# Performance work log

Measured on AMD Instinct MI355X. Metric: run time of the kernel, lower is better.

## Reference

```python
import jax, jax.numpy as jnp
import numpy as np

B, T, C = 1, 2048, 1024
H, D = 16, 64  # n_head, head_size (n_query_groups == n_head -> plain MHA)


def build_rope_cache(seq_len, n_elem, base=10000):
    theta = 1.0 / (base ** (jnp.arange(0, n_elem, 2, dtype=jnp.float32) / n_elem))
    idx_theta = jnp.outer(jnp.arange(seq_len, dtype=jnp.float32), theta)
    idx_theta = jnp.concatenate([idx_theta, idx_theta], axis=-1)  # torch .repeat(1, 2)
    return jnp.cos(idx_theta), jnp.sin(idx_theta)


def apply_rope(x, cos, sin):
    d = x.shape[-1]
    x1, x2 = x[..., : d // 2], x[..., d // 2 :]
    rotated = jnp.concatenate([-x2, x1], axis=-1)
    return x * cos + rotated * sin


def fastmax_attention(q, k, v):
    """Fastmax: first-order Taylor approx of softmax attention, causal, O(n*d^2).
    score(i,j) = 1 + q_i . k_j (temperature=1, zero RPE, no dropout);
    out_i = sum_{j<=i} score*v_j / sum_{j<=i} score, via causal cumulative sums."""
    n = q.shape[2]
    kcum = jnp.cumsum(k, axis=2)                                       # (B,H,T,D)
    kvcum = jnp.cumsum(jnp.einsum('bhnd,bhne->bhnde', k, v), axis=2)   # (B,H,T,D,D)
    den = jnp.arange(1, n + 1, dtype=q.dtype) + jnp.einsum('bhnd,bhnd->bhn', q, kcum)
    num = jnp.cumsum(v, axis=2) + jnp.einsum('bhnd,bhnde->bhne', q, kvcum)
    return num / den[..., None]


def setup_inputs() -> dict:
    key = jax.random.key(0)
    k1, k2, k3 = jax.random.split(key, 3)
    scale = 0.02
    x = jax.random.normal(k1, (B, T, C), dtype=jnp.float32)
    w_attn = jax.random.normal(k2, (3 * H * D, C), dtype=jnp.float32) * scale
    w_proj = jax.random.normal(k3, (C, H * D), dtype=jnp.float32) * scale
    cos, sin = build_rope_cache(T, D)
    return {"x": x, "w_attn": w_attn, "w_proj": w_proj, "cos": cos, "sin": sin}


def reference(x, w_attn, w_proj, cos, sin):
    Bx, Tx, Cx = x.shape
    qkv = x @ w_attn.T                                  # (B,T,3HD)
    qkv = qkv.reshape(Bx, Tx, H, 3, D).transpose(0, 2, 3, 1, 4)  # (B,H,3,T,D)
    q, k, v = qkv[:, :, 0], qkv[:, :, 1], qkv[:, :, 2]
    q = apply_rope(q, cos, sin)
    k = apply_rope(k, cos, sin)
    y = fastmax_attention(q, k, v)                      # (B,H,T,D)
    y = y.transpose(0, 2, 1, 3).reshape(Bx, Tx, H * D)
    return y @ w_proj.T
```

## Files before the change

### kernel.cpp

```cpp
#include <hip/hip_runtime.h>

#define T_LEN 2048
#define C_DIM 1024
#define H_NUM 16
#define D_DIM 64
#define QKV_N (3 * H_NUM * D_DIM)
#define L_CHK 64
#define NC (T_LEN / L_CHK)

typedef _Float16 h8 __attribute__((ext_vector_type(8)));
typedef _Float16 h4 __attribute__((ext_vector_type(4)));
typedef float f32x4 __attribute__((ext_vector_type(4)));

__global__ __launch_bounds__(256) void split3_f16(
    const float* __restrict__ x, _Float16* __restrict__ xh,
    _Float16* __restrict__ xl, const float* __restrict__ wa,
    _Float16* __restrict__ wah, _Float16* __restrict__ wal,
    const float* __restrict__ wp, _Float16* __restrict__ wph) {
  int i = (blockIdx.x * 256 + threadIdx.x) * 8;
  const float* src;
  _Float16 *dh, *dl = nullptr;
  int base;
  if (i < 2097152) {
    src = x; dh = xh; dl = xl; base = i;
  } else if (i < 2097152 + 3145728) {
    src = wa; dh = wah; dl = wal; base = i - 2097152;
  } else {
    src = wp; dh = wph; base = i - 5242880;
  }
  float4 a = *(const float4*)(src + base);
  float4 b = *(const float4*)(src + base + 4);
  float v[8] = {a.x, a.y, a.z, a.w, b.x, b.y, b.z, b.w};
  h8 hv, lv;
#pragma unroll
  for (int j = 0; j < 8; ++j) {
    float s = v[j] * 64.f;
    _Float16 h = (_Float16)s;
    hv[j] = h;
    lv[j] = (_Float16)(s - (float)h);
  }
  *(h8*)(dh + base) = hv;
  if (dl) *(h8*)(dl + base) = lv;
}

__device__ __forceinline__ void split8(float4 a, float4 b, h8& hi, h8& lo) {
  float v[8] = {a.x, a.y, a.z, a.w, b.x, b.y, b.z, b.w};
#pragma unroll
  for (int m = 0; m < 8; ++m) {
    _Float16 hh = (_Float16)v[m];
    hi[m] = hh;
    lo[m] = (_Float16)(v[m] - (float)hh);
  }
}

template <int BN, bool ROPE, bool SPLIT3>
__global__ __launch_bounds__(256) void gemm_nt_f16(
    const _Float16* __restrict__ Ah, const _Float16* __restrict__ Al,
    const _Float16* __restrict__ Bh, const _Float16* __restrict__ Bl,
    float* __restrict__ C, const float* __restrict__ cosb,
    const float* __restrict__ sinb, _Float16* __restrict__ qh_,
    _Float16* __restrict__ ql_, _Float16* __restrict__ kh_,
    _Float16* __restrict__ kl_, _Float16* __restrict__ kTh_,
    _Float16* __restrict__ kTl_, _Float16* __restrict__ vTh_,
    _Float16* __restrict__ vTl_, int M, int N, int K, float outscale) {
  constexpr int NJ = BN / 32;
  constexpr int NARR = SPLIT3 ? 2 : 1;
  constexpr int GEMM_BYTES = (64 * 64 * 2 + BN * 64 * 2) * NARR;
  constexpr int ROPE_BYTES = ROPE ? (2 * 64 * 32 * 4 + 2 * 64 * 64 * 4) : 0;
  constexpr int SMEM_BYTES = GEMM_BYTES > ROPE_BYTES ? GEMM_BYTES : ROPE_BYTES;
  __shared__ __align__(16) char smem[SMEM_BYTES];
  _Float16* sAh = (_Float16*)smem;
  _Float16* sAl = sAh + 64 * 64;
  _Float16* sBh = sAh + 64 * 64 * NARR;
  _Float16* sBl = sBh + BN * 64;
  const int tid = threadIdx.x;
  const int wave = tid >> 6;
  const int lane = tid & 63;
  const int bm = blockIdx.y * 64;
  const int bn = blockIdx.x * BN;
  const int wm = wave >> 1;
  const int wn = wave & 1;
  const int srow = lane >> 3;
  const int sblk = ((lane & 7) ^ srow) * 8;
  const int quad = lane >> 4;
  const int lrow = lane & 15;

  f32x4 acc[2][NJ];
#pragma unroll
  for (int i = 0; i < 2; ++i)
#pragma unroll
    for (int j = 0; j < NJ; ++j) acc[i][j] = (f32x4){0.f, 0.f, 0.f, 0.f};

  for (int k0 = 0; k0 < K; k0 += 64) {
#pragma unroll
    for (int it = 0; it < 2; ++it) {
      const int ch = wave + it * 4;
      const int row = ch * 8 + srow;
      const _Float16* ga = Ah + (size_t)(bm + row) * K + k0 + sblk;
      __builtin_amdgcn_global_load_lds(
          (const __attribute__((address_space(1))) void*)ga,
          (__attribute__((address_space(3))) void*)(sAh + ch * 512), 16, 0, 0);
      if constexpr (SPLIT3) {
        const _Float16* gb = Al + (size_t)(bm + row) * K + k0 + sblk;
        __builtin_amdgcn_global_load_lds(
            (const __attribute__((address_space(1))) void*)gb,
            (__attribute__((address_space(3))) void*)(sAl + ch * 512), 16, 0,
            0);
      }
    }
#pragma unroll
    for (int it = 0; it < BN / 32; ++it) {
      const int ch = wave + it * 4;
      const int row = ch * 8 + srow;
      const _Float16* ga = Bh + (size_t)(bn + row) * K + k0 + sblk;
      __builtin_amdgcn_global_load_lds(
          (const __attribute__((address_space(1))) void*)ga,
          (__attribute__((address_space(3))) void*)(sBh + ch * 512), 16, 0, 0);
      if constexpr (SPLIT3) {
        const _Float16* gb = Bl + (size_t)(bn + row) * K + k0 + sblk;
        __builtin_amdgcn_global_load_lds(
            (const __attribute__((address_space(1))) void*)gb,
            (__attribute__((address_space(3))) void*)(sBl + ch * 512), 16, 0,
            0);
      }
    }
    __syncthreads();
#pragma unroll
    for (int kk = 0; kk < 2; ++kk) {
      h8 ah[2], al[2], bh[NJ], bl[NJ];
#pragma unroll
      for (int i = 0; i < 2; ++i) {
        const int row = wm * 32 + i * 16 + lrow;
        const int ra = row * 64 + (((kk * 4 + quad) ^ (row & 7)) * 8);
        ah[i] = *(const h8*)&sAh[ra];
        if constexpr (SPLIT3) al[i] = *(const h8*)&sAl[ra];
      }
#pragma unroll
      for (int j = 0; j < NJ; ++j) {
        const int row = wn * (BN / 2) + j * 16 + lrow;
        const int rb = row * 64 + (((kk * 4 + quad) ^ (row & 7)) * 8);
        bh[j] = *(const h8*)&sBh[rb];
        if constexpr (SPLIT3) bl[j] = *(const h8*)&sBl[rb];
      }
#pragma unroll
      for (int i = 0; i < 2; ++i)
#pragma unroll
        for (int j = 0; j < NJ; ++j) {
          acc[i][j] = __builtin_amdgcn_mfma_f32_16x16x32_f16(
              ah[i], bh[j], acc[i][j], 0, 0, 0);
          if constexpr (SPLIT3) {
            acc[i][j] = __builtin_amdgcn_mfma_f32_16x16x32_f16(
                ah[i], bl[j], acc[i][j], 0, 0, 0);
            acc[i][j] = __builtin_amdgcn_mfma_f32_16x16x32_f16(
                al[i], bh[j], acc[i][j], 0, 0, 0);
          }
        }
    }
    __syncthreads();
  }
  if constexpr (!ROPE) {
#pragma unroll
    for (int i = 0; i < 2; ++i) {
      const int rbase = bm + wm * 32 + i * 16 + quad * 4;
#pragma unroll
      for (int j = 0; j < NJ; ++j) {
        const int col = bn + wn * (BN / 2) + j * 16 + lrow;
#pragma unroll
        for (int r = 0; r < 4; ++r)
          C[(size_t)(rbase + r) * N + col] = acc[i][j][r] * outscale;
      }
    }
  } else {
    float* cs = (float*)smem;
    float* sn = cs + 2048;
    float* bounce = sn + 2048;
    {
      const int el = tid * 8;
      const int t = el >> 5, d0 = el & 31;
      const float* gc = &cosb[(size_t)(bm + t) * D_DIM + d0];
      const float* gs = &sinb[(size_t)(bm + t) * D_DIM + d0];
      *(float4*)&cs[t * 32 + d0] = *(const float4*)gc;
      *(float4*)&cs[t * 32 + d0 + 4] = *(const float4*)(gc + 4);
      *(float4*)&sn[t * 32 + d0] = *(const float4*)gs;
      *(float4*)&sn[t * 32 + d0 + 4] = *(const float4*)(gs + 4);
    }
    __syncthreads();
    const int colbase = bn + wn * 64;
    const int type = (colbase >> 6) % 3;
    const int head = colbase / 192;
    const size_t hb = (size_t)head * T_LEN * D_DIM;
    float fv[2][4][4];
#pragma unroll
    for (int i = 0; i < 2; ++i)
#pragma unroll
      for (int r = 0; r < 4; ++r) {
        const int tloc = wm * 32 + i * 16 + quad * 4 + r;
#pragma unroll
        for (int j = 0; j < 4; ++j) {
          const int d32 = (j & 1) * 16 + lrow;
          float val = acc[i][j][r] * outscale;
          if (type < 2) {
            float rotv =
                ((j < 2) ? -acc[i][j + 2][r] : acc[i][j - 2][r]) * outscale;
            val = val * cs[tloc * 32 + d32] + rotv * sn[tloc * 32 + d32];
          }
          fv[i][r][j] = val;
        }
      }
    if (type < 2) {
      _Float16* dh = (type == 0 ? qh_ : kh_) + hb;
      _Float16* dl = (type == 0 ? ql_ : kl_) + hb;
#pragma unroll
      for (int i = 0; i < 2; ++i)
#pragma unroll
        for (int r = 0; r < 4; ++r) {
          const size_t trow =
              (size_t)(bm + wm * 32 + i * 16 + quad * 4 + r) * D_DIM;
#pragma unroll
          for (int j = 0; j < 4; ++j) {
            const int d = j * 16 + lrow;
            float f = fv[i][r][j];
            _Float16 hh = (_Float16)f;
            dh[trow + d] = hh;
            dl[trow + d] = (_Float16)(f - (float)hh);
          }
        }
    }
    const bool doT = (type >= 1);
    _Float16* th = (type == 1 ? kTh_ : vTh_) + hb;
    _Float16* tl = (type == 1 ? kTl_ : vTl_) + hb;
    float* myb = bounce + wn * 4096;
    if (doT) {
#pragma unroll
      for (int i = 0; i < 2; ++i)
#pragma unroll
        for (int r = 0; r < 4; ++r) {
          const int tloc = wm * 32 + i * 16 + quad * 4 + r;
#pragma unroll
          for (int j = 0; j < 4; ++j) {
            const int d = j * 16 + lrow;
            myb[tloc * 64 + (d ^ tloc)] = fv[i][r][j];
          }
        }
    }
    __syncthreads();
    if (doT) {
      const int lt = wm * 64 + lane;
      const int e = lt >> 1;
      const int tg0 = (lt & 1) * 32;
#pragma unroll
      for (int s8 = 0; s8 < 4; ++s8) {
        h8 hv, lv;
#pragma unroll
        for (int s = 0; s < 8; ++s) {
          const int t = tg0 + s8 * 8 + s;
          float f = myb[t * 64 + (e ^ t)];
          _Float16 hh = (_Float16)f;
          hv[s] = hh;
          lv[s] = (_Float16)(f - (float)hh);
        }
        *(h8*)&th[(size_t)e * T_LEN + bm + tg0 + s8 * 8] = hv;
        *(h8*)&tl[(size_t)e * T_LEN + bm + tg0 + s8 * 8] = lv;
      }
    }
  }
}

__global__ __launch_bounds__(256) void chunk_kvT(
    const _Float16* __restrict__ kTh, const _Float16* __restrict__ kTl,
    const _Float16* __restrict__ vTh, const _Float16* __restrict__ vTl,
    float* __restrict__ kvchunk, float* __restrict__ kschunk,
    float* __restrict__ vschunk) {
  const int blk = blockIdx.x;
  const int h = blk / NC, c = blk % NC;
  const int tid = threadIdx.x;
  const int wave = tid >> 6, lane = tid & 63;
  const int quad = lane >> 4, lrow = lane & 15;
  const size_t hb = (size_t)h * D_DIM * T_LEN;
  const int tb = c * L_CHK;
  h8 avh[2], avl[2];
  {
    const _Float16* pa = vTh + hb + (size_t)(wave * 16 + lrow) * T_LEN + tb +
                         quad * 8;
    const _Float16* pal = vTl + hb + (size_t)(wave * 16 + lrow) * T_LEN + tb +
                          quad * 8;
    avh[0] = *(const h8*)pa;
    avh[1] = *(const h8*)(pa + 32);
    avl[0] = *(const h8*)pal;
    avl[1] = *(const h8*)(pal + 32);
  }
  f32x4 accv[4];
#pragma unroll
  for (int dt = 0; dt < 4; ++dt) accv[dt] = (f32x4){0.f, 0.f, 0.f, 0.f};
#pragma unroll
  for (int dt = 0; dt < 4; ++dt) {
    const _Float16* pb = kTh + hb + (size_t)(dt * 16 + lrow) * T_LEN + tb +
                         quad * 8;
    const _Float16* pbl = kTl + hb + (size_t)(dt * 16 + lrow) * T_LEN + tb +
                          quad * 8;
#pragma unroll
    for (int ks = 0; ks < 2; ++ks) {
      h8 bh = *(const h8*)(pb + ks * 32);
      h8 bl = *(const h8*)(pbl + ks * 32);
      accv[dt] = __builtin_amdgcn_mfma_f32_16x16x32_f16(avh[ks], bh, accv[dt],
                                                        0, 0, 0);
      accv[dt] = __builtin_amdgcn_mfma_f32_16x16x32_f16(avh[ks], bl, accv[dt],
                                                        0, 0, 0);
      accv[dt] = __builtin_amdgcn_mfma_f32_16x16x32_f16(avl[ks], bh, accv[dt],
                                                        0, 0, 0);
    }
  }
  float* ob = kvchunk + (size_t)blk * (D_DIM * D_DIM);
#pragma unroll
  for (int dt = 0; dt < 4; ++dt)
#pragma unroll
    for (int r = 0; r < 4; ++r)
      ob[(wave * 16 + quad * 4 + r) * D_DIM + dt * 16 + lrow] = accv[dt][r];
  if (tid < 64) {
    const _Float16* p = kTh + hb + (size_t)tid * T_LEN + tb;
    const _Float16* pl = kTl + hb + (size_t)tid * T_LEN + tb;
    float s = 0.f;
#pragma unroll
    for (int i = 0; i < 8; ++i) {
      h8 a = *(const h8*)(p + i * 8), b = *(const h8*)(pl + i * 8);
#pragma unroll
      for (int m = 0; m < 8; ++m) s += (float)a[m] + (float)b[m];
    }
    kschunk[(size_t)blk * D_DIM + tid] = s;
  } else if (tid < 128) {
    const int e = tid - 64;
    const _Float16* p = vTh + hb + (size_t)e * T_LEN + tb;
    const _Float16* pl = vTl + hb + (size_t)e * T_LEN + tb;
    float s = 0.f;
#pragma unroll
    for (int i = 0; i < 8; ++i) {
      h8 a = *(const h8*)(p + i * 8), b = *(const h8*)(pl + i * 8);
#pragma unroll
      for (int m = 0; m < 8; ++m) s += (float)a[m] + (float)b[m];
    }
    vschunk[(size_t)blk * D_DIM + e] = s;
  }
}

__global__ __launch_bounds__(256) void scan_fused(
    const float* __restrict__ kvchunk, float* __restrict__ kvpref,
    const float* __restrict__ kschunk, const float* __restrict__ vschunk,
    float* __restrict__ kspref, float* __restrict__ vspref) {
  int b = blockIdx.x;
  int tid = threadIdx.x;
  if (b < 256) {
    int gid = b * 256 + tid;
    int h = gid >> 12;
    int de = gid & 4095;
    float vals[NC];
#pragma unroll
    for (int c = 0; c < NC; ++c)
      vals[c] = kvchunk[((size_t)(h * NC + c) << 12) + de];
    float run = 0.f;
#pragma unroll
    for (int c = 0; c < NC; ++c) {
      kvpref[((size_t)(h * NC + c) << 12) + de] = run;
      run += vals[c];
    }
  } else {
    int gid = (b - 256) * 256 + tid;
    int h = gid >> 6, d = gid & 63;
    float kv_[NC], vv_[NC];
#pragma unroll
    for (int c = 0; c < NC; ++c) {
      size_t idx = (size_t)(h * NC + c) * 64 + d;
      kv_[c] = kschunk[idx];
      vv_[c] = vschunk[idx];
    }
    float rk = 0.f, rv = 0.f;
#pragma unroll
    for (int c = 0; c < NC; ++c) {
      size_t idx = (size_t)(h * NC + c) * 64 + d;
      kspref[idx] = rk;
      vspref[idx] = rv;
      rk += kv_[c];
      rv += vv_[c];
    }
  }
}

__global__ __launch_bounds__(256) void attn_mfma(
    const _Float16* __restrict__ qh, const _Float16* __restrict__ ql,
    const _Float16* __restrict__ kh, const _Float16* __restrict__ kl,
    const _Float16* __restrict__ vTh, const _Float16* __restrict__ vTl,
    const float* __restrict__ kvpref, const float* __restrict__ kspref,
    const float* __restrict__ vspref, _Float16* __restrict__ yh) {
  __shared__ __align__(16) _Float16 sS[2][4][16 * 64];
  const int blk = blockIdx.x;
  const int h = blk / NC, c = blk % NC;
  const int tid = threadIdx.x;
  const int wave = tid >> 6, lane = tid & 63;
  const int quad = lane >> 4, lrow = lane & 15;
  const size_t hb = (size_t)h * T_LEN * D_DIM;
  const size_t hbT = (size_t)h * D_DIM * T_LEN;
  const int t0 = c * L_CHK;
  const f32x4 z4 = {0.f, 0.f, 0.f, 0.f};
  h8 aqh[2], aql[2];
  {
    const _Float16* pq =
        qh + hb + (size_t)(t0 + wave * 16 + lrow) * D_DIM + quad * 8;
    const _Float16* pql =
        ql + hb + (size_t)(t0 + wave * 16 + lrow) * D_DIM + quad * 8;
    aqh[0] = *(const h8*)pq;
    aqh[1] = *(const h8*)(pq + 32);
    aql[0] = *(const h8*)pql;
    aql[1] = *(const h8*)(pql + 32);
  }
  f32x4 sacc[4];
#pragma unroll
  for (int jt = 0; jt < 4; ++jt) sacc[jt] = z4;
#pragma unroll
  for (int jt = 0; jt < 4; ++jt) {
    const _Float16* pk =
        kh + hb + (size_t)(t0 + jt * 16 + lrow) * D_DIM + quad * 8;
    const _Float16* pkl =
        kl + hb + (size_t)(t0 + jt * 16 + lrow) * D_DIM + quad * 8;
#pragma unroll
    for (int ks = 0; ks < 2; ++ks) {
      h8 bh = *(const h8*)(pk + ks * 32);
      h8 bl = *(const h8*)(pkl + ks * 32);
      sacc[jt] = __builtin_amdgcn_mfma_f32_16x16x32_f16(aqh[ks], bh, sacc[jt],
                                                        0, 0, 0);
      sacc[jt] = __builtin_amdgcn_mfma_f32_16x16x32_f16(aqh[ks], bl, sacc[jt],
                                                        0, 0, 0);
      sacc[jt] = __builtin_amdgcn_mfma_f32_16x16x32_f16(aql[ks], bh, sacc[jt],
                                                        0, 0, 0);
    }
  }
  _Float16* shp = &sS[0][wave][0];
  _Float16* slp = &sS[1][wave][0];
#pragma unroll
  for (int jt = 0; jt < 4; ++jt)
#pragma unroll
    for (int r = 0; r < 4; ++r) {
      const int row = quad * 4 + r;
      const int j = jt * 16 + lrow;
      const int rglob = wave * 16 + row;
      float s = (j <= rglob) ? (sacc[jt][r] + 1.f) : 0.f;
      _Float16 hh = (_Float16)s;
      const int adr = row * 64 + ((((j >> 3) ^ (row & 7)) << 3) | (j & 7));
      shp[adr] = hh;
      slp[adr] = (_Float16)(s - (float)hh);
    }
  h8 ash[2], asl[2];
#pragma unroll
  for (int ks = 0; ks < 2; ++ks) {
    const int adr = lrow * 64 + (((ks * 4 + quad) ^ (lrow & 7)) << 3);
    ash[ks] = *(const h8*)&shp[adr];
    asl[ks] = *(const h8*)&slp[adr];
  }
  h8 ones;
#pragma unroll
  for (int m = 0; m < 8; ++m) ones[m] = (_Float16)1.0f;
  f32x4 rs = z4;
#pragma unroll
  for (int ks = 0; ks < 2; ++ks) {
    rs = __builtin_amdgcn_mfma_f32_16x16x32_f16(ash[ks], ones, rs, 0, 0, 0);
    rs = __builtin_amdgcn_mfma_f32_16x16x32_f16(asl[ks], ones, rs, 0, 0, 0);
  }
  f32x4 oacc[4];
#pragma unroll
  for (int et = 0; et < 4; ++et) oacc[et] = z4;
#pragma unroll
  for (int et = 0; et < 4; ++et) {
    const _Float16* pv =
        vTh + hbT + (size_t)(et * 16 + lrow) * T_LEN + t0 + quad * 8;
    const _Float16* pvl =
        vTl + hbT + (size_t)(et * 16 + lrow) * T_LEN + t0 + quad * 8;
#pragma unroll
    for (int ks = 0; ks < 2; ++ks) {
      h8 bh = *(const h8*)(pv + ks * 32);
      h8 bl = *(const h8*)(pvl + ks * 32);
      oacc[et] = __builtin_amdgcn_mfma_f32_16x16x32_f16(ash[ks], bh, oacc[et],
                                                        0, 0, 0);
      oacc[et] = __builtin_amdgcn_mfma_f32_16x16x32_f16(ash[ks], bl, oacc[et],
                                                        0, 0, 0);
      oacc[et] = __builtin_amdgcn_mfma_f32_16x16x32_f16(asl[ks], bh, oacc[et],
                                                        0, 0, 0);
    }
  }
  const float* kvp = kvpref + (size_t)blk * (D_DIM * D_DIM);
#pragma unroll
  for (int et = 0; et < 4; ++et) {
#pragma unroll
    for (int ks = 0; ks < 2; ++ks) {
      const float* pb = kvp + (et * 16 + lrow) * D_DIM + ks * 32 + quad * 8;
      float4 b0 = *(const float4*)pb;
      float4 b1 = *(const float4*)(pb + 4);
      h8 bh, bl;
      split8(b0, b1, bh, bl);
      oacc[et] = __builtin_amdgcn_mfma_f32_16x16x32_f16(aqh[ks], bh, oacc[et],
                                                        0, 0, 0);
      oacc[et] = __builtin_amdgcn_mfma_f32_16x16x32_f16(aqh[ks], bl, oacc[et],
                                                        0, 0, 0);
      oacc[et] = __builtin_amdgcn_mfma_f32_16x16x32_f16(aql[ks], bh, oacc[et],
                                                        0, 0, 0);
    }
  }
  const float* ksp = kspref + (size_t)blk * D_DIM;
  f32x4 kacc = z4;
#pragma unroll
  for (int ks = 0; ks < 2; ++ks) {
    const float* pb = ksp + ks * 32 + quad * 8;
    float4 b0 = *(const float4*)pb;
    float4 b1 = *(const float4*)(pb + 4);
    h8 bh, bl;
    split8(b0, b1, bh, bl);
    kacc = __builtin_amdgcn_mfma_f32_16x16x32_f16(aqh[ks], bh, kacc, 0, 0, 0);
    kacc = __builtin_amdgcn_mfma_f32_16x16x32_f16(aqh[ks], bl, kacc, 0, 0, 0);
    kacc = __builtin_amdgcn_mfma_f32_16x16x32_f16(aql[ks], bh, kacc, 0, 0, 0);
  }
  const float* vsp = vspref + (size_t)blk * D_DIM;
#pragma unroll
  for (int r = 0; r < 4; ++r) {
    const int row = wave * 16 + quad * 4 + r;
    const float den = (float)(c * L_CHK) + rs[r] + kacc[r];
    const float inv = 1.f / den;
    const size_t ybase = (size_t)(t0 + row) * (H_NUM * D_DIM) + h * D_DIM;
#pragma unroll
    for (int et = 0; et < 4; ++et) {
      const int e = et * 16 + lrow;
      const float num = oacc[et][r] + vsp[e];
      yh[ybase + e] = (_Float16)(num * inv);
    }
  }
}

extern "C" void kernel_launch(void* const* d_in, const int* in_sizes, int n_in,
                              void* d_out, int out_size, void* d_ws,
                              size_t ws_size, hipStream_t stream) {
  const float* x = (const float*)d_in[0];
  const float* w_attn = (const float*)d_in[1];
  const float* w_proj = (const float*)d_in[2];
  const float* cosb = (const float*)d_in[3];
  const float* sinb = (const float*)d_in[4];
  float* out = (float*)d_out;

  char* ws = (char*)d_ws;
  const size_t MB = 1048576;
  float* kvchunk = (float*)ws;
  float* kvpref = (float*)(ws + 8 * MB);
  _Float16* qh = (_Float16*)(ws + 16 * MB);
  _Float16* ql = (_Float16*)(ws + 20 * MB);
  _Float16* kh = (_Float16*)(ws + 24 * MB);
  _Float16* kl = (_Float16*)(ws + 28 * MB);
  _Float16* kTh = (_Float16*)(ws + 32 * MB);
  _Float16* kTl = (_Float16*)(ws + 36 * MB);
  _Float16* vTh = (_Float16*)(ws + 40 * MB);
  _Float16* vTl = (_Float16*)(ws + 44 * MB);
  _Float16* xh = (_Float16*)(ws + 48 * MB);
  _Float16* xl = (_Float16*)(ws + 52 * MB);
  _Float16* yh = (_Float16*)(ws + 48 * MB);
  _Float16* wah = (_Float16*)(ws + 56 * MB);
  _Float16* wal = (_Float16*)(ws + 62 * MB);
  float* kschunk = (float*)(ws + 56 * MB);
  float* vschunk = (float*)(ws + 56 * MB + 131072);
  float* kspref = (float*)(ws + 56 * MB + 262144);
  float* vspref = (float*)(ws + 56 * MB + 393216);
  _Float16* wph = (_Float16*)(ws + 68 * MB);

  split3_f16<<<3072, 256, 0, stream>>>(x, xh, xl, w_attn, wah, wal, w_proj,
                                       wph);

  {
    dim3 grid(QKV_N / 128, T_LEN / 64);
    gemm_nt_f16<128, true, true><<<grid, 256, 0, stream>>>(
        xh, xl, wah, wal, nullptr, cosb, sinb, qh, ql, kh, kl, kTh, kTl, vTh,
        vTl, T_LEN, QKV_N, C_DIM, 1.f / 4096.f);
  }
  chunk_kvT<<<H_NUM * NC, 256, 0, stream>>>(kTh, kTl, vTh, vTl, kvchunk,
                                            kschunk, vschunk);
  scan_fused<<<260, 256, 0, stream>>>(kvchunk, kvpref, kschunk, vschunk,
                                      kspref, vspref);
  attn_mfma<<<H_NUM * NC, 256, 0, stream>>>(qh, ql, kh, kl, vTh, vTl, kvpref,
                                            kspref, vspref, yh);
  {
    dim3 grid(C_DIM / 64, T_LEN / 64);
    gemm_nt_f16<64, false, false><<<grid, 256, 0, stream>>>(
        yh, nullptr, wph, nullptr, out, nullptr, nullptr, nullptr, nullptr,
        nullptr, nullptr, nullptr, nullptr, nullptr, nullptr, T_LEN, C_DIM,
        C_DIM, 1.f / 64.f);
  }
}
```

Before: 168.1 us.

## Enlarge QKV GEMM tile to 128x128 and rework RoPE/transpose epilogue

The QKV projection GEMM now uses a BM template parameter and runs with 128x128 tiles, halving the number of blocks and raising per-block operand reuse of the split-f16 A/B tiles. The RoPE epilogue is reworked for the larger tile: cos/sin staging covers 128 rows, and each wave gets its own 64x64 bounce buffer for the K/V transpose, with an extra barrier. Launch bounds request 2 blocks per SM. The cost is more accumulator registers (16 f32x4 per thread with triple MFMA), 64KB of LDS for the epilogue, and only 384 blocks, which may hurt occupancy and load balance.

Result: no change. 168.3 us (+0.2%).

```diff
diff --git a/kernel.cpp b/kernel.cpp
--- a/kernel.cpp
+++ b/kernel.cpp
@@ -53,8 +53,8 @@
   }
 }
 
-template <int BN, bool ROPE, bool SPLIT3>
-__global__ __launch_bounds__(256) void gemm_nt_f16(
+template <int BM, int BN, bool ROPE, bool SPLIT3>
+__global__ __launch_bounds__(256, 2) void gemm_nt_f16(
     const _Float16* __restrict__ Ah, const _Float16* __restrict__ Al,
     const _Float16* __restrict__ Bh, const _Float16* __restrict__ Bl,
     float* __restrict__ C, const float* __restrict__ cosb,
@@ -63,20 +63,21 @@
     _Float16* __restrict__ kl_, _Float16* __restrict__ kTh_,
     _Float16* __restrict__ kTl_, _Float16* __restrict__ vTh_,
     _Float16* __restrict__ vTl_, int M, int N, int K, float outscale) {
+  constexpr int MI = BM / 32;
   constexpr int NJ = BN / 32;
   constexpr int NARR = SPLIT3 ? 2 : 1;
-  constexpr int GEMM_BYTES = (64 * 64 * 2 + BN * 64 * 2) * NARR;
-  constexpr int ROPE_BYTES = ROPE ? (2 * 64 * 32 * 4 + 2 * 64 * 64 * 4) : 0;
+  constexpr int GEMM_BYTES = (BM * 64 * 2 + BN * 64 * 2) * NARR;
+  constexpr int ROPE_BYTES = ROPE ? 65536 : 0;
   constexpr int SMEM_BYTES = GEMM_BYTES > ROPE_BYTES ? GEMM_BYTES : ROPE_BYTES;
   __shared__ __align__(16) char smem[SMEM_BYTES];
   _Float16* sAh = (_Float16*)smem;
-  _Float16* sAl = sAh + 64 * 64;
-  _Float16* sBh = sAh + 64 * 64 * NARR;
+  _Float16* sAl = sAh + BM * 64;
+  _Float16* sBh = sAh + BM * 64 * NARR;
   _Float16* sBl = sBh + BN * 64;
   const int tid = threadIdx.x;
   const int wave = tid >> 6;
   const int lane = tid & 63;
-  const int bm = blockIdx.y * 64;
+  const int bm = blockIdx.y * BM;
   const int bn = blockIdx.x * BN;
   const int wm = wave >> 1;
   const int wn = wave & 1;
@@ -85,15 +86,15 @@
   const int quad = lane >> 4;
   const int lrow = lane & 15;
 
-  f32x4 acc[2][NJ];
-#pragma unroll
-  for (int i = 0; i < 2; ++i)
+  f32x4 acc[MI][NJ];
+#pragma unroll
+  for (int i = 0; i < MI; ++i)
 #pragma unroll
     for (int j = 0; j < NJ; ++j) acc[i][j] = (f32x4){0.f, 0.f, 0.f, 0.f};
 
   for (int k0 = 0; k0 < K; k0 += 64) {
 #pragma unroll
-    for (int it = 0; it < 2; ++it) {
+    for (int it = 0; it < MI; ++it) {
       const int ch = wave + it * 4;
       const int row = ch * 8 + srow;
       const _Float16* ga = Ah + (size_t)(bm + row) * K + k0 + sblk;
@@ -109,7 +110,7 @@
       }
     }
 #pragma unroll
-    for (int it = 0; it < BN / 32; ++it) {
+    for (int it = 0; it < NJ; ++it) {
       const int ch = wave + it * 4;
       const int row = ch * 8 + srow;
       const _Float16* ga = Bh + (size_t)(bn + row) * K + k0 + sblk;
@@ -127,10 +128,10 @@
     __syncthreads();
 #pragma unroll
     for (int kk = 0; kk < 2; ++kk) {
-      h8 ah[2], al[2], bh[NJ], bl[NJ];
-#pragma unroll
-      for (int i = 0; i < 2; ++i) {
-        const int row = wm * 32 + i * 16 + lrow;
+      h8 ah[MI], al[MI], bh[NJ], bl[NJ];
+#pragma unroll
+      for (int i = 0; i < MI; ++i) {
+        const int row = wm * (BM / 2) + i * 16 + lrow;
         const int ra = row * 64 + (((kk * 4 + quad) ^ (row & 7)) * 8);
         ah[i] = *(const h8*)&sAh[ra];
         if constexpr (SPLIT3) al[i] = *(const h8*)&sAl[ra];
@@ -143,7 +144,7 @@
         if constexpr (SPLIT3) bl[j] = *(const h8*)&sBl[rb];
       }
 #pragma unroll
-      for (int i = 0; i < 2; ++i)
+      for (int i = 0; i < MI; ++i)
 #pragma unroll
         for (int j = 0; j < NJ; ++j) {
           acc[i][j] = __builtin_amdgcn_mfma_f32_16x16x32_f16(
@@ -160,8 +161,8 @@
   }
   if constexpr (!ROPE) {
 #pragma unroll
-    for (int i = 0; i < 2; ++i) {
-      const int rbase = bm + wm * 32 + i * 16 + quad * 4;
+    for (int i = 0; i < MI; ++i) {
+      const int rbase = bm + wm * (BM / 2) + i * 16 + quad * 4;
 #pragma unroll
       for (int j = 0; j < NJ; ++j) {
         const int col = bn + wn * (BN / 2) + j * 16 + lrow;
@@ -172,29 +173,31 @@
     }
   } else {
     float* cs = (float*)smem;
-    float* sn = cs + 2048;
-    float* bounce = sn + 2048;
+    float* sn = cs + 4096;
     {
-      const int el = tid * 8;
-      const int t = el >> 5, d0 = el & 31;
+      const int t = tid >> 1, d0 = (tid & 1) * 16;
       const float* gc = &cosb[(size_t)(bm + t) * D_DIM + d0];
       const float* gs = &sinb[(size_t)(bm + t) * D_DIM + d0];
       *(float4*)&cs[t * 32 + d0] = *(const float4*)gc;
       *(float4*)&cs[t * 32 + d0 + 4] = *(const float4*)(gc + 4);
+      *(float4*)&cs[t * 32 + d0 + 8] = *(const float4*)(gc + 8);
+      *(float4*)&cs[t * 32 + d0 + 12] = *(const float4*)(gc + 12);
       *(float4*)&sn[t * 32 + d0] = *(const float4*)gs;
       *(float4*)&sn[t * 32 + d0 + 4] = *(const float4*)(gs + 4);
+      *(float4*)&sn[t * 32 + d0 + 8] = *(const float4*)(gs + 8);
+      *(float4*)&sn[t * 32 + d0 + 12] = *(const float4*)(gs + 12);
     }
     __syncthreads();
     const int colbase = bn + wn * 64;
     const int type = (colbase >> 6) % 3;
     const int head = colbase / 192;
     const size_t hb = (size_t)head * T_LEN * D_DIM;
-    float fv[2][4][4];
-#pragma unroll
-    for (int i = 0; i < 2; ++i)
+    float fv[4][4][4];
+#pragma unroll
+    for (int i = 0; i < 4; ++i)
 #pragma unroll
       for (int r = 0; r < 4; ++r) {
-        const int tloc = wm * 32 + i * 16 + quad * 4 + r;
+        const int tloc = wm * 64 + i * 16 + quad * 4 + r;
 #pragma unroll
         for (int j = 0; j < 4; ++j) {
           const int d32 = (j & 1) * 16 + lrow;
@@ -211,11 +214,11 @@
       _Float16* dh = (type == 0 ? qh_ : kh_) + hb;
       _Float16* dl = (type == 0 ? ql_ : kl_) + hb;
 #pragma unroll
-      for (int i = 0; i < 2; ++i)
+      for (int i = 0; i < 4; ++i)
 #pragma unroll
         for (int r = 0; r < 4; ++r) {
           const size_t trow =
-              (size_t)(bm + wm * 32 + i * 16 + quad * 4 + r) * D_DIM;
+              (size_t)(bm + wm * 64 + i * 16 + quad * 4 + r) * D_DIM;
 #pragma unroll
           for (int j = 0; j < 4; ++j) {
             const int d = j * 16 + lrow;
@@ -229,38 +232,38 @@
     const bool doT = (type >= 1);
     _Float16* th = (type == 1 ? kTh_ : vTh_) + hb;
     _Float16* tl = (type == 1 ? kTl_ : vTl_) + hb;
-    float* myb = bounce + wn * 4096;
+    float* myb = (float*)smem + wave * 4096;
+    __syncthreads();
     if (doT) {
 #pragma unroll
-      for (int i = 0; i < 2; ++i)
+      for (int i = 0; i < 4; ++i)
 #pragma unroll
         for (int r = 0; r < 4; ++r) {
-          const int tloc = wm * 32 + i * 16 + quad * 4 + r;
+          const int tl64 = i * 16 + quad * 4 + r;
 #pragma unroll
           for (int j = 0; j < 4; ++j) {
             const int d = j * 16 + lrow;
-            myb[tloc * 64 + (d ^ tloc)] = fv[i][r][j];
+            myb[tl64 * 64 + (d ^ tl64)] = fv[i][r][j];
           }
         }
     }
     __syncthreads();
     if (doT) {
-      const int lt = wm * 64 + lane;
-      const int e = lt >> 1;
-      const int tg0 = (lt & 1) * 32;
-#pragma unroll
-      for (int s8 = 0; s8 < 4; ++s8) {
+      const int e = lane;
+      const size_t obase = (size_t)e * T_LEN + bm + wm * 64;
+#pragma unroll
+      for (int s8 = 0; s8 < 8; ++s8) {
         h8 hv, lv;
 #pragma unroll
         for (int s = 0; s < 8; ++s) {
-          const int t = tg0 + s8 * 8 + s;
+          const int t = s8 * 8 + s;
           float f = myb[t * 64 + (e ^ t)];
           _Float16 hh = (_Float16)f;
           hv[s] = hh;
           lv[s] = (_Float16)(f - (float)hh);
         }
-        *(h8*)&th[(size_t)e * T_LEN + bm + tg0 + s8 * 8] = hv;
-        *(h8*)&tl[(size_t)e * T_LEN + bm + tg0 + s8 * 8] = lv;
+        *(h8*)&th[obase + s8 * 8] = hv;
+        *(h8*)&tl[obase + s8 * 8] = lv;
       }
     }
   }
@@ -568,8 +571,8 @@
                                        wph);
 
   {
-    dim3 grid(QKV_N / 128, T_LEN / 64);
-    gemm_nt_f16<128, true, true><<<grid, 256, 0, stream>>>(
+    dim3 grid(QKV_N / 128, T_LEN / 128);
+    gemm_nt_f16<128, 128, true, true><<<grid, 256, 0, stream>>>(
         xh, xl, wah, wal, nullptr, cosb, sinb, qh, ql, kh, kl, kTh, kTl, vTh,
         vTl, T_LEN, QKV_N, C_DIM, 1.f / 4096.f);
   }
@@ -581,7 +584,7 @@
                                             kspref, vspref, yh);
   {
     dim3 grid(C_DIM / 64, T_LEN / 64);
-    gemm_nt_f16<64, false, false><<<grid, 256, 0, stream>>>(
+    gemm_nt_f16<64, 64, false, false><<<grid, 256, 0, stream>>>(
         yh, nullptr, wph, nullptr, out, nullptr, nullptr, nullptr, nullptr,
         nullptr, nullptr, nullptr, nullptr, nullptr, nullptr, T_LEN, C_DIM,
         C_DIM, 1.f / 64.f);
```

## Drop low-half split for V and store KV prefix in fp16

Applied to the files above, without the earlier changes.

Removes the lo-part fp16 split for V: the QKV GEMM epilogue no longer writes vTl, and chunk_kvT and attn_mfma drop the corresponding MFMAs and loads. The KV prefix state from the scan is stored as single fp16 instead of fp32, which removes the split8 conversion and the extra MFMAs in attention. The rope cos/sin shared-memory stride is padded from 32 to 36, presumably to reduce LDS bank conflicts. This lowers memory traffic and matrix work but reduces accuracy, since V and the accumulated KV state lose precision, and large accumulated prefix values may lose accuracy in fp16.

Measured after the change: 161.2 us. -4.1%, faster.

```diff
diff --git a/kernel.cpp b/kernel.cpp
--- a/kernel.cpp
+++ b/kernel.cpp
@@ -62,11 +62,11 @@
     _Float16* __restrict__ ql_, _Float16* __restrict__ kh_,
     _Float16* __restrict__ kl_, _Float16* __restrict__ kTh_,
     _Float16* __restrict__ kTl_, _Float16* __restrict__ vTh_,
-    _Float16* __restrict__ vTl_, int M, int N, int K, float outscale) {
+    int M, int N, int K, float outscale) {
   constexpr int NJ = BN / 32;
   constexpr int NARR = SPLIT3 ? 2 : 1;
   constexpr int GEMM_BYTES = (64 * 64 * 2 + BN * 64 * 2) * NARR;
-  constexpr int ROPE_BYTES = ROPE ? (2 * 64 * 32 * 4 + 2 * 64 * 64 * 4) : 0;
+  constexpr int ROPE_BYTES = ROPE ? (2 * 64 * 36 * 4 + 2 * 64 * 64 * 4) : 0;
   constexpr int SMEM_BYTES = GEMM_BYTES > ROPE_BYTES ? GEMM_BYTES : ROPE_BYTES;
   __shared__ __align__(16) char smem[SMEM_BYTES];
   _Float16* sAh = (_Float16*)smem;
@@ -172,17 +172,17 @@
     }
   } else {
     float* cs = (float*)smem;
-    float* sn = cs + 2048;
-    float* bounce = sn + 2048;
+    float* sn = cs + 2304;
+    float* bounce = sn + 2304;
     {
       const int el = tid * 8;
       const int t = el >> 5, d0 = el & 31;
       const float* gc = &cosb[(size_t)(bm + t) * D_DIM + d0];
       const float* gs = &sinb[(size_t)(bm + t) * D_DIM + d0];
-      *(float4*)&cs[t * 32 + d0] = *(const float4*)gc;
-      *(float4*)&cs[t * 32 + d0 + 4] = *(const float4*)(gc + 4);
-      *(float4*)&sn[t * 32 + d0] = *(const float4*)gs;
-      *(float4*)&sn[t * 32 + d0 + 4] = *(const float4*)(gs + 4);
+      *(float4*)&cs[t * 36 + d0] = *(const float4*)gc;
+      *(float4*)&cs[t * 36 + d0 + 4] = *(const float4*)(gc + 4);
+      *(float4*)&sn[t * 36 + d0] = *(const float4*)gs;
+      *(float4*)&sn[t * 36 + d0 + 4] = *(const float4*)(gs + 4);
     }
     __syncthreads();
     const int colbase = bn + wn * 64;
@@ -202,7 +202,7 @@
           if (type < 2) {
             float rotv =
                 ((j < 2) ? -acc[i][j + 2][r] : acc[i][j - 2][r]) * outscale;
-            val = val * cs[tloc * 32 + d32] + rotv * sn[tloc * 32 + d32];
+            val = val * cs[tloc * 36 + d32] + rotv * sn[tloc * 36 + d32];
           }
           fv[i][r][j] = val;
         }
@@ -228,7 +228,7 @@
     }
     const bool doT = (type >= 1);
     _Float16* th = (type == 1 ? kTh_ : vTh_) + hb;
-    _Float16* tl = (type == 1 ? kTl_ : vTl_) + hb;
+    _Float16* tl = kTl_ + hb;
     float* myb = bounce + wn * 4096;
     if (doT) {
 #pragma unroll
@@ -260,7 +260,8 @@
           lv[s] = (_Float16)(f - (float)hh);
         }
         *(h8*)&th[(size_t)e * T_LEN + bm + tg0 + s8 * 8] = hv;
-        *(h8*)&tl[(size_t)e * T_LEN + bm + tg0 + s8 * 8] = lv;
+        if (type == 1)
+          *(h8*)&tl[(size_t)e * T_LEN + bm + tg0 + s8 * 8] = lv;
       }
     }
   }
@@ -268,9 +269,8 @@
 
 __global__ __launch_bounds__(256) void chunk_kvT(
     const _Float16* __restrict__ kTh, const _Float16* __restrict__ kTl,
-    const _Float16* __restrict__ vTh, const _Float16* __restrict__ vTl,
-    float* __restrict__ kvchunk, float* __restrict__ kschunk,
-    float* __restrict__ vschunk) {
+    const _Float16* __restrict__ vTh, float* __restrict__ kvchunk,
+    float* __restrict__ kschunk, float* __restrict__ vschunk) {
   const int blk = blockIdx.x;
   const int h = blk / NC, c = blk % NC;
   const int tid = threadIdx.x;
@@ -278,16 +278,12 @@
   const int quad = lane >> 4, lrow = lane & 15;
   const size_t hb = (size_t)h * D_DIM * T_LEN;
   const int tb = c * L_CHK;
-  h8 avh[2], avl[2];
+  h8 avh[2];
   {
     const _Float16* pa = vTh + hb + (size_t)(wave * 16 + lrow) * T_LEN + tb +
                          quad * 8;
-    const _Float16* pal = vTl + hb + (size_t)(wave * 16 + lrow) * T_LEN + tb +
-                          quad * 8;
     avh[0] = *(const h8*)pa;
     avh[1] = *(const h8*)(pa + 32);
-    avl[0] = *(const h8*)pal;
-    avl[1] = *(const h8*)(pal + 32);
   }
   f32x4 accv[4];
 #pragma unroll
@@ -296,17 +292,10 @@
   for (int dt = 0; dt < 4; ++dt) {
     const _Float16* pb = kTh + hb + (size_t)(dt * 16 + lrow) * T_LEN + tb +
                          quad * 8;
-    const _Float16* pbl = kTl + hb + (size_t)(dt * 16 + lrow) * T_LEN + tb +
-                          quad * 8;
 #pragma unroll
     for (int ks = 0; ks < 2; ++ks) {
       h8 bh = *(const h8*)(pb + ks * 32);
-      h8 bl = *(const h8*)(pbl + ks * 32);
       accv[dt] = __builtin_amdgcn_mfma_f32_16x16x32_f16(avh[ks], bh, accv[dt],
-                                                        0, 0, 0);
-      accv[dt] = __builtin_amdgcn_mfma_f32_16x16x32_f16(avh[ks], bl, accv[dt],
-                                                        0, 0, 0);
-      accv[dt] = __builtin_amdgcn_mfma_f32_16x16x32_f16(avl[ks], bh, accv[dt],
                                                         0, 0, 0);
     }
   }
@@ -330,20 +319,19 @@
   } else if (tid < 128) {
     const int e = tid - 64;
     const _Float16* p = vTh + hb + (size_t)e * T_LEN + tb;
-    const _Float16* pl = vTl + hb + (size_t)e * T_LEN + tb;
     float s = 0.f;
 #pragma unroll
     for (int i = 0; i < 8; ++i) {
-      h8 a = *(const h8*)(p + i * 8), b = *(const h8*)(pl + i * 8);
-#pragma unroll
-      for (int m = 0; m < 8; ++m) s += (float)a[m] + (float)b[m];
+      h8 a = *(const h8*)(p + i * 8);
+#pragma unroll
+      for (int m = 0; m < 8; ++m) s += (float)a[m];
     }
     vschunk[(size_t)blk * D_DIM + e] = s;
   }
 }
 
 __global__ __launch_bounds__(256) void scan_fused(
-    const float* __restrict__ kvchunk, float* __restrict__ kvpref,
+    const float* __restrict__ kvchunk, _Float16* __restrict__ kvph,
     const float* __restrict__ kschunk, const float* __restrict__ vschunk,
     float* __restrict__ kspref, float* __restrict__ vspref) {
   int b = blockIdx.x;
@@ -359,7 +347,7 @@
     float run = 0.f;
 #pragma unroll
     for (int c = 0; c < NC; ++c) {
-      kvpref[((size_t)(h * NC + c) << 12) + de] = run;
+      kvph[((size_t)(h * NC + c) << 12) + de] = (_Float16)run;
       run += vals[c];
     }
   } else {
@@ -387,9 +375,9 @@
 __global__ __launch_bounds__(256) void attn_mfma(
     const _Float16* __restrict__ qh, const _Float16* __restrict__ ql,
     const _Float16* __restrict__ kh, const _Float16* __restrict__ kl,
-    const _Float16* __restrict__ vTh, const _Float16* __restrict__ vTl,
-    const float* __restrict__ kvpref, const float* __restrict__ kspref,
-    const float* __restrict__ vspref, _Float16* __restrict__ yh) {
+    const _Float16* __restrict__ vTh, const _Float16* __restrict__ kvph,
+    const float* __restrict__ kspref, const float* __restrict__ vspref,
+    _Float16* __restrict__ yh) {
   __shared__ __align__(16) _Float16 sS[2][4][16 * 64];
   const int blk = blockIdx.x;
   const int h = blk / NC, c = blk % NC;
@@ -470,35 +458,22 @@
   for (int et = 0; et < 4; ++et) {
     const _Float16* pv =
         vTh + hbT + (size_t)(et * 16 + lrow) * T_LEN + t0 + quad * 8;
-    const _Float16* pvl =
-        vTl + hbT + (size_t)(et * 16 + lrow) * T_LEN + t0 + quad * 8;
 #pragma unroll
     for (int ks = 0; ks < 2; ++ks) {
       h8 bh = *(const h8*)(pv + ks * 32);
-      h8 bl = *(const h8*)(pvl + ks * 32);
       oacc[et] = __builtin_amdgcn_mfma_f32_16x16x32_f16(ash[ks], bh, oacc[et],
                                                         0, 0, 0);
-      oacc[et] = __builtin_amdgcn_mfma_f32_16x16x32_f16(ash[ks], bl, oacc[et],
-                                                        0, 0, 0);
       oacc[et] = __builtin_amdgcn_mfma_f32_16x16x32_f16(asl[ks], bh, oacc[et],
                                                         0, 0, 0);
     }
   }
-  const float* kvp = kvpref + (size_t)blk * (D_DIM * D_DIM);
+  const _Float16* kvp = kvph + ((size_t)blk << 12);
 #pragma unroll
   for (int et = 0; et < 4; ++et) {
 #pragma unroll
     for (int ks = 0; ks < 2; ++ks) {
-      const float* pb = kvp + (et * 16 + lrow) * D_DIM + ks * 32 + quad * 8;
-      float4 b0 = *(const float4*)pb;
-      float4 b1 = *(const float4*)(pb + 4);
-      h8 bh, bl;
-      split8(b0, b1, bh, bl);
+      h8 bh = *(const h8*)&kvp[(et * 16 + lrow) * D_DIM + ks * 32 + quad * 8];
       oacc[et] = __builtin_amdgcn_mfma_f32_16x16x32_f16(aqh[ks], bh, oacc[et],
-                                                        0, 0, 0);
-      oacc[et] = __builtin_amdgcn_mfma_f32_16x16x32_f16(aqh[ks], bl, oacc[et],
-                                                        0, 0, 0);
-      oacc[et] = __builtin_amdgcn_mfma_f32_16x16x32_f16(aql[ks], bh, oacc[et],
                                                         0, 0, 0);
     }
   }
@@ -544,7 +519,7 @@
   char* ws = (char*)d_ws;
   const size_t MB = 1048576;
   float* kvchunk = (float*)ws;
-  float* kvpref = (float*)(ws + 8 * MB);
+  _Float16* kvph = (_Float16*)(ws + 8 * MB);
   _Float16* qh = (_Float16*)(ws + 16 * MB);
   _Float16* ql = (_Float16*)(ws + 20 * MB);
   _Float16* kh = (_Float16*)(ws + 24 * MB);
@@ -552,7 +527,6 @@
   _Float16* kTh = (_Float16*)(ws + 32 * MB);
   _Float16* kTl = (_Float16*)(ws + 36 * MB);
   _Float16* vTh = (_Float16*)(ws + 40 * MB);
-  _Float16* vTl = (_Float16*)(ws + 44 * MB);
   _Float16* xh = (_Float16*)(ws + 48 * MB);
   _Float16* xl = (_Float16*)(ws + 52 * MB);
   _Float16* yh = (_Float16*)(ws + 48 * MB);
@@ -571,19 +545,19 @@
     dim3 grid(QKV_N / 128, T_LEN / 64);
     gemm_nt_f16<128, true, true><<<grid, 256, 0, stream>>>(
         xh, xl, wah, wal, nullptr, cosb, sinb, qh, ql, kh, kl, kTh, kTl, vTh,
-        vTl, T_LEN, QKV_N, C_DIM, 1.f / 4096.f);
-  }
-  chunk_kvT<<<H_NUM * NC, 256, 0, stream>>>(kTh, kTl, vTh, vTl, kvchunk,
-                                            kschunk, vschunk);
-  scan_fused<<<260, 256, 0, stream>>>(kvchunk, kvpref, kschunk, vschunk,
+        T_LEN, QKV_N, C_DIM, 1.f / 4096.f);
+  }
+  chunk_kvT<<<H_NUM * NC, 256, 0, stream>>>(kTh, kTl, vTh, kvchunk, kschunk,
+                                            vschunk);
+  scan_fused<<<260, 256, 0, stream>>>(kvchunk, kvph, kschunk, vschunk,
                                       kspref, vspref);
-  attn_mfma<<<H_NUM * NC, 256, 0, stream>>>(qh, ql, kh, kl, vTh, vTl, kvpref,
+  attn_mfma<<<H_NUM * NC, 256, 0, stream>>>(qh, ql, kh, kl, vTh, kvph,
                                             kspref, vspref, yh);
   {
     dim3 grid(C_DIM / 64, T_LEN / 64);
     gemm_nt_f16<64, false, false><<<grid, 256, 0, stream>>>(
         yh, nullptr, wph, nullptr, out, nullptr, nullptr, nullptr, nullptr,
-        nullptr, nullptr, nullptr, nullptr, nullptr, nullptr, T_LEN, C_DIM,
-        C_DIM, 1.f / 64.f);
-  }
-}
+        nullptr, nullptr, nullptr, nullptr, nullptr, T_LEN, C_DIM, C_DIM,
+        1.f / 64.f);
+  }
+}
```
